# Optimization experiments

Hardware: AMD Instinct MI355X
Metric: run time of the kernel (lower is better)

Reference implementation:

```python
import jax, jax.numpy as jnp
import numpy as np

B_BOUND = 3.0
K = 10
SCALE_DIM = 8
TOTAL_DIM = 16
HID = 50
N = 262144
TD = TOTAL_DIM - SCALE_DIM  # transform_dim


def setup_inputs() -> dict:
    key = jax.random.key(0)
    ks = jax.random.split(key, 7)
    s = 0.1  # small init so softmax/softplus params stay well-conditioned
    return {
        "x": jax.random.normal(ks[0], (N, TOTAL_DIM), dtype=jnp.float32),
        "w0": s * jax.random.normal(ks[1], (SCALE_DIM, HID), dtype=jnp.float32),
        "b0": jnp.zeros((HID,), jnp.float32),
        "w1": s * jax.random.normal(ks[2], (HID, HID), dtype=jnp.float32),
        "b1": jnp.zeros((HID,), jnp.float32),
        "ww": s * jax.random.normal(ks[3], (HID, TD * K), dtype=jnp.float32),
        "bw": jnp.zeros((TD * K,), jnp.float32),
        "wh": s * jax.random.normal(ks[4], (HID, TD * K), dtype=jnp.float32),
        "bh": jnp.zeros((TD * K,), jnp.float32),
        "wd": s * jax.random.normal(ks[5], (HID, TD * (K - 1)), dtype=jnp.float32),
        "bd": jnp.zeros((TD * (K - 1),), jnp.float32),
    }


def _spline_forward(x, w0, b0, w1, b1, ww, bw, wh, bh, wd, bd):
    B = B_BOUND
    zd = x[:, :SCALE_DIM]          # conditioner input [N, d]
    u = x[:, SCALE_DIM:]           # values to transform [N, D]
    n, D = u.shape

    h = jnp.tanh(zd @ w0 + b0)
    h = jnp.tanh(h @ w1 + b1)

    theta_w = jax.nn.softmax((2.0 * B * (h @ ww + bw)).reshape(n, D, K), axis=-1)
    theta_h = jax.nn.softmax((2.0 * B * (h @ wh + bh)).reshape(n, D, K), axis=-1)
    theta_d = jax.nn.softplus((h @ wd + bd).reshape(n, D, K - 1))

    # Bin edges in [-B, B] via cumsum of normalized widths/heights
    xe = jnp.concatenate(
        [jnp.full((n, D, 1), -B, u.dtype), -B + 2.0 * B * jnp.cumsum(theta_w, axis=-1)], axis=-1)  # [n,D,K+1]
    ye = jnp.concatenate(
        [jnp.full((n, D, 1), -B, u.dtype), -B + 2.0 * B * jnp.cumsum(theta_h, axis=-1)], axis=-1)
    # Knot derivatives: boundary derivatives fixed to 1 (linear tails)
    ones = jnp.ones((n, D, 1), u.dtype)
    d = jnp.concatenate([ones, theta_d, ones], axis=-1)  # [n,D,K+1]

    widths = xe[..., 1:] - xe[..., :-1]
    heights = ye[..., 1:] - ye[..., :-1]

    inside = (u > -B) & (u < B)
    uc = jnp.clip(u, -B, B)
    # per-element bin search
    idx = jnp.clip(jnp.sum((uc[..., None] >= xe[..., :-1]).astype(jnp.int32), axis=-1) - 1, 0, K - 1)
    idx = idx[..., None]
    take = lambda a: jnp.take_along_axis(a, idx, axis=-1)[..., 0]

    xk, yk = take(xe[..., :-1]), take(ye[..., :-1])
    wk, hk = take(widths), take(heights)
    dk, dk1 = take(d[..., :-1]), take(d[..., 1:])

    sk = hk / wk
    xi = (uc - xk) / wk
    om = 1.0 - xi
    denom = sk + (dk1 + dk - 2.0 * sk) * xi * om
    y = yk + hk * (sk * xi * xi + dk * xi * om) / denom
    logdet = 2.0 * jnp.log(sk) + jnp.log(dk1 * xi * xi + 2.0 * sk * xi * om + dk * om * om) - 2.0 * jnp.log(denom)

    zD = jnp.where(inside, y, u)
    ld = jnp.where(inside, logdet, 0.0)
    return jnp.concatenate([zd, zD], axis=1), jnp.sum(ld)


def reference(x, w0, b0, w1, b1, ww, bw, wh, bh, wd, bd):
    return _spline_forward(x, w0, b0, w1, b1, ww, bw, wh, bh, wd, bd)
```

## Files before the change

kernel.cpp:

```cpp
#include <hip/hip_runtime.h>

#define NROWS 262144
#define KK 10
#define BB 3.0f
#define SROW 260
#define SEGF16 (16 * SROW)

typedef _Float16 v8h __attribute__((ext_vector_type(8)));
typedef _Float16 v4h __attribute__((ext_vector_type(4)));
typedef float v4f __attribute__((ext_vector_type(4)));

#define W0_OFF 0
#define W1_OFF 256
#define WC_OFF 768
#define FRAG_TOTAL 2816
#define SLOTS_OFF (FRAG_TOTAL * 4)

__device__ __forceinline__ float fast_tanh(float a) {
    float e = __expf(2.0f * a);
    return 1.0f - __fdividef(2.0f, e + 1.0f);
}

__global__ __launch_bounds__(256) void nsf_prep(
    const float* __restrict__ w0, const float* __restrict__ b0,
    const float* __restrict__ w1, const float* __restrict__ b1,
    const float* __restrict__ ww, const float* __restrict__ bw,
    const float* __restrict__ wh, const float* __restrict__ bh,
    const float* __restrict__ wd, const float* __restrict__ bd,
    v8h* __restrict__ wsv, float* __restrict__ wsf)
{
    const int t = blockIdx.x * 256 + threadIdx.x;
    if (t < 64) wsf[SLOTS_OFF + t] = 0.0f;
    if (t >= FRAG_TOTAL) return;

    v8h v;
    #pragma unroll
    for (int j = 0; j < 8; ++j) v[j] = (_Float16)0.0f;

    if (t < W1_OFF) {
        const int tile = t >> 6, lane = t & 63, q = lane >> 4, n = tile * 16 + (lane & 15);
        if (n < 50) {
            #pragma unroll
            for (int j = 0; j < 8; ++j) {
                const int k = q * 8 + j;
                if (k < 8)       v[j] = (_Float16)w0[k * 50 + n];
                else if (k == 8) v[j] = (_Float16)b0[n];
            }
        }
    } else if (t < WC_OFF) {
        int p = t - W1_OFF;
        const int step = p >> 8; p &= 255;
        const int tile = p >> 6, lane = p & 63, q = lane >> 4, n = tile * 16 + (lane & 15);
        if (n < 50) {
            #pragma unroll
            for (int j = 0; j < 8; ++j) {
                const int k = step * 32 + q * 8 + j;
                if (k < 50)       v[j] = (_Float16)w1[k * 50 + n];
                else if (k == 50) v[j] = (_Float16)b1[n];
            }
        }
    } else {
        int p = t - WC_OFF;
        const int step = p >> 10; p &= 1023;
        const int tile = p >> 6, lane = p & 63, q = lane >> 4;
        const int cp = tile * 16 + (lane & 15);
        const int d = cp >> 5, jj = cp & 31;
        #pragma unroll
        for (int j = 0; j < 8; ++j) {
            const int k = step * 32 + q * 8 + j;
            float val = 0.0f;
            if (k < 50) {
                if (jj < 10)      val = ww[k * 80 + d * 10 + jj];
                else if (jj < 20) val = wh[k * 80 + d * 10 + (jj - 10)];
                else if (jj < 29) val = wd[k * 72 + d * 9 + (jj - 20)];
            } else if (k == 50) {
                if (jj < 10)      val = bw[d * 10 + jj];
                else if (jj < 20) val = bh[d * 10 + (jj - 10)];
                else if (jj < 29) val = bd[d * 9 + (jj - 20)];
            }
            v[j] = (_Float16)val;
        }
    }
    wsv[t] = v;
}

__global__ __launch_bounds__(64, 2) void nsf_main(
    const float* __restrict__ x,
    const v8h* __restrict__ wsv,
    float* __restrict__ out, float* __restrict__ slots)
{
    __shared__ __align__(16) _Float16 smem[2 * SEGF16];
    const int lane = threadIdx.x & 63;
    const int q = lane >> 4, l15 = lane & 15;
    _Float16* segA = &smem[0];
    _Float16* segB = &smem[SEGF16];
    const int R0 = blockIdx.x * 32;

    const float4* xv = (const float4*)x;
    float4* ov = (float4*)out;

    const float uA0 = x[(R0 + l15) * 16 + 8 + q];
    const float uA1 = x[(R0 + l15) * 16 + 12 + q];
    const float uB0 = x[(R0 + 16 + l15) * 16 + 8 + q];
    const float uB1 = x[(R0 + 16 + l15) * 16 + 12 + q];

    {
        const int gg = R0 + (lane >> 1);
        const int part = lane & 1;
        ov[gg * 4 + part] = xv[gg * 4 + part];
    }

    v8h aA, aB;
    #pragma unroll
    for (int j = 0; j < 8; ++j) { aA[j] = (_Float16)0.0f; aB[j] = (_Float16)0.0f; }
    if (lane < 16) {
        const float4 f0 = xv[(R0 + lane) * 4 + 0];
        const float4 f1 = xv[(R0 + lane) * 4 + 1];
        aA[0] = (_Float16)f0.x; aA[1] = (_Float16)f0.y; aA[2] = (_Float16)f0.z; aA[3] = (_Float16)f0.w;
        aA[4] = (_Float16)f1.x; aA[5] = (_Float16)f1.y; aA[6] = (_Float16)f1.z; aA[7] = (_Float16)f1.w;
        const float4 g0 = xv[(R0 + 16 + lane) * 4 + 0];
        const float4 g1 = xv[(R0 + 16 + lane) * 4 + 1];
        aB[0] = (_Float16)g0.x; aB[1] = (_Float16)g0.y; aB[2] = (_Float16)g0.z; aB[3] = (_Float16)g0.w;
        aB[4] = (_Float16)g1.x; aB[5] = (_Float16)g1.y; aB[6] = (_Float16)g1.z; aB[7] = (_Float16)g1.w;
    }
    if (q == 1) { aA[0] = (_Float16)1.0f; aB[0] = (_Float16)1.0f; }

    #pragma unroll
    for (int t = 0; t < 4; ++t) {
        const v8h b = wsv[W0_OFF + t * 64 + lane];
        v4f cA = __builtin_amdgcn_mfma_f32_16x16x32_f16(aA, b, (v4f)(0.0f), 0, 0, 0);
        v4f cB = __builtin_amdgcn_mfma_f32_16x16x32_f16(aB, b, (v4f)(0.0f), 0, 0, 0);
        const int n = t * 16 + l15;
        #pragma unroll
        for (int rg = 0; rg < 4; ++rg) {
            segA[(q * 4 + rg) * 72 + n] = (_Float16)fast_tanh(cA[rg]);
            segB[(q * 4 + rg) * 72 + n] = (_Float16)fast_tanh(cB[rg]);
        }
    }

    v8h A0A, A1A, A0B, A1B;
    {
        A0A = *(const v8h*)&segA[l15 * 72 + q * 8];
        A1A = *(const v8h*)&segA[l15 * 72 + 32 + q * 8];
        A0B = *(const v8h*)&segB[l15 * 72 + q * 8];
        A1B = *(const v8h*)&segB[l15 * 72 + 32 + q * 8];
        if (q == 2) { A1A[2] = (_Float16)1.0f; A1B[2] = (_Float16)1.0f; }
        #pragma unroll
        for (int t = 0; t < 4; ++t) {
            const v8h bf0 = wsv[W1_OFF + t * 64 + lane];
            const v8h bf1 = wsv[W1_OFF + 256 + t * 64 + lane];
            v4f cA = __builtin_amdgcn_mfma_f32_16x16x32_f16(A0A, bf0, (v4f)(0.0f), 0, 0, 0);
            cA = __builtin_amdgcn_mfma_f32_16x16x32_f16(A1A, bf1, cA, 0, 0, 0);
            v4f cB = __builtin_amdgcn_mfma_f32_16x16x32_f16(A0B, bf0, (v4f)(0.0f), 0, 0, 0);
            cB = __builtin_amdgcn_mfma_f32_16x16x32_f16(A1B, bf1, cB, 0, 0, 0);
            const int n = t * 16 + l15;
            #pragma unroll
            for (int rg = 0; rg < 4; ++rg) {
                segA[(q * 4 + rg) * 72 + n] = (_Float16)fast_tanh(cA[rg]);
                segB[(q * 4 + rg) * 72 + n] = (_Float16)fast_tanh(cB[rg]);
            }
        }
    }

    {
        A0A = *(const v8h*)&segA[l15 * 72 + q * 8];
        A1A = *(const v8h*)&segA[l15 * 72 + 32 + q * 8];
        A0B = *(const v8h*)&segB[l15 * 72 + q * 8];
        A1B = *(const v8h*)&segB[l15 * 72 + 32 + q * 8];
        if (q == 2) { A1A[2] = (_Float16)1.0f; A1B[2] = (_Float16)1.0f; }
        #pragma unroll 2
        for (int t = 0; t < 16; ++t) {
            const v8h bf0 = wsv[WC_OFF + t * 64 + lane];
            const v8h bf1 = wsv[WC_OFF + 1024 + t * 64 + lane];
            v4f cA = __builtin_amdgcn_mfma_f32_16x16x32_f16(A0A, bf0, (v4f)(0.0f), 0, 0, 0);
            cA = __builtin_amdgcn_mfma_f32_16x16x32_f16(A1A, bf1, cA, 0, 0, 0);
            v4f cB = __builtin_amdgcn_mfma_f32_16x16x32_f16(A0B, bf0, (v4f)(0.0f), 0, 0, 0);
            cB = __builtin_amdgcn_mfma_f32_16x16x32_f16(A1B, bf1, cB, 0, 0, 0);
            const int cp = t * 16 + l15;
            #pragma unroll
            for (int rg = 0; rg < 4; ++rg) {
                segA[(q * 4 + rg) * SROW + cp] = (_Float16)cA[rg];
                segB[(q * 4 + rg) * SROW + cp] = (_Float16)cB[rg];
            }
        }
    }

    float ldacc = 0.0f;
    #pragma unroll 1
    for (int task = 0; task < 4; ++task) {
        const int tile = task >> 1, tt = task & 1;
        const int d = q + tt * 4;
        const int g = R0 + tile * 16 + l15;
        const float ud = (tile == 0) ? (tt == 0 ? uA0 : uA1) : (tt == 0 ? uB0 : uB1);
        const _Float16* sg = (tile == 0) ? segA : segB;
        const int base = l15 * SROW + d * 32;

        float vals[32];
        #pragma unroll
        for (int blk = 0; blk < 8; ++blk) {
            const v4h p = *(const v4h*)&sg[base + blk * 4];
            vals[4 * blk + 0] = (float)p[0];
            vals[4 * blk + 1] = (float)p[1];
            vals[4 * blk + 2] = (float)p[2];
            vals[4 * blk + 3] = (float)p[3];
        }

        float mw = vals[0];
        #pragma unroll
        for (int i = 1; i < KK; ++i) mw = fmaxf(mw, vals[i]);
        float sw = 0.0f;
        #pragma unroll
        for (int i = 0; i < KK; ++i) { vals[i] = __expf(6.0f * (vals[i] - mw)); sw += vals[i]; }
        const float invw = __fdividef(1.0f, sw);

        float mh = vals[10];
        #pragma unroll
        for (int i = 1; i < KK; ++i) mh = fmaxf(mh, vals[10 + i]);
        float sh = 0.0f;
        #pragma unroll
        for (int i = 0; i < KK; ++i) { vals[10 + i] = __expf(6.0f * (vals[10 + i] - mh)); sh += vals[10 + i]; }
        const float invh = __fdividef(1.0f, sh);

        float sp[KK - 1];
        #pragma unroll
        for (int i = 0; i < KK - 1; ++i) {
            const float v = vals[20 + i];
            sp[i] = fmaxf(v, 0.0f) + __logf(1.0f + __expf(-fabsf(v)));
        }

        const float uc = fminf(fmaxf(ud, -BB), BB);
        const bool inside = (ud > -BB) && (ud < BB);

        float cw = 0.0f, ch = 0.0f;
        float xprev = -BB, yprev = -BB, dprev = 1.0f;
        float xk = -BB, yk = -BB, wk = 1.0f, hk2 = 1.0f, dk = 1.0f, dk1 = 1.0f;
        #pragma unroll
        for (int i = 0; i < KK; ++i) {
            cw += vals[i] * invw;
            ch += vals[10 + i] * invh;
            const float xnext = fmaf(6.0f, cw, -BB);
            const float ynext = fmaf(6.0f, ch, -BB);
            const float dnext = (i == KK - 1) ? 1.0f : sp[i];
            const bool c = (i == 0) || (uc >= xprev);
            if (c) { xk = xprev; yk = yprev; wk = xnext - xprev; hk2 = ynext - yprev; dk = dprev; dk1 = dnext; }
            xprev = xnext; yprev = ynext; dprev = dnext;
        }

        const float sk = __fdividef(hk2, wk);
        const float xi = __fdividef(uc - xk, wk);
        const float om = 1.0f - xi;
        const float denom = sk + (dk1 + dk - 2.0f * sk) * xi * om;
        const float ynum = sk * xi * xi + dk * xi * om;
        const float yv = yk + hk2 * __fdividef(ynum, denom);
        const float larg = dk1 * xi * xi + 2.0f * sk * xi * om + dk * om * om;
        const float ldet = 2.0f * __logf(sk) + __logf(larg) - 2.0f * __logf(denom);

        out[g * 16 + 8 + d] = inside ? yv : ud;
        ldacc += inside ? ldet : 0.0f;
    }

    #pragma unroll
    for (int off = 32; off > 0; off >>= 1) ldacc += __shfl_down(ldacc, off);
    if (lane == 0) atomicAdd(&slots[blockIdx.x & 63], ldacc);
}

__global__ void nsf_finish(const float* __restrict__ slots, float* __restrict__ ldp) {
    float v = slots[threadIdx.x];
    #pragma unroll
    for (int off = 32; off > 0; off >>= 1) v += __shfl_down(v, off);
    if (threadIdx.x == 0) *ldp = v;
}

extern "C" void kernel_launch(void* const* d_in, const int* in_sizes, int n_in,
                              void* d_out, int out_size, void* d_ws, size_t ws_size,
                              hipStream_t stream) {
    const float* x  = (const float*)d_in[0];
    const float* w0 = (const float*)d_in[1];
    const float* b0 = (const float*)d_in[2];
    const float* w1 = (const float*)d_in[3];
    const float* b1 = (const float*)d_in[4];
    const float* ww = (const float*)d_in[5];
    const float* bw = (const float*)d_in[6];
    const float* wh = (const float*)d_in[7];
    const float* bh = (const float*)d_in[8];
    const float* wd = (const float*)d_in[9];
    const float* bd = (const float*)d_in[10];

    float* out = (float*)d_out;
    float* ldp = out + (size_t)NROWS * 16;
    v8h* wsv = (v8h*)d_ws;
    float* wsf = (float*)d_ws;
    float* slots = wsf + SLOTS_OFF;

    hipLaunchKernelGGL(nsf_prep, dim3((FRAG_TOTAL + 255) / 256), dim3(256), 0, stream,
                       w0, b0, w1, b1, ww, bw, wh, bh, wd, bd, wsv, wsf);
    hipLaunchKernelGGL(nsf_main, dim3(NROWS / 32), dim3(64), 0, stream,
                       x, wsv, out, slots);
    hipLaunchKernelGGL(nsf_finish, dim3(1), dim3(64), 0, stream, slots, ldp);
}
```

Before: 169.7 us.

## Defer softplus to selected knots, merge logs, fold finish kernel into main

The spline loop now carries the raw derivative logits and applies softplus only to the two selected knots, not to all nine. Boundary knots use a sentinel whose softplus equals 1. The three log calls are merged into one log of a product, and divisions become reciprocal multiplies. The separate finish kernel is replaced by a last-block-done counter inside the main kernel, which saves a launch. The costs are an extra global atomic per block and some risk of precision loss or overflow in the combined log argument.

```diff
diff --git a/kernel.cpp b/kernel.cpp
--- a/kernel.cpp
+++ b/kernel.cpp
@@ -5,6 +5,8 @@
 #define BB 3.0f
 #define SROW 260
 #define SEGF16 (16 * SROW)
+#define NBLOCKS (NROWS / 32)
+#define SENT 0.54132485f
 
 typedef _Float16 v8h __attribute__((ext_vector_type(8)));
 typedef _Float16 v4h __attribute__((ext_vector_type(4)));
@@ -19,6 +21,10 @@
 __device__ __forceinline__ float fast_tanh(float a) {
     float e = __expf(2.0f * a);
     return 1.0f - __fdividef(2.0f, e + 1.0f);
+}
+
+__device__ __forceinline__ float softplus1(float v) {
+    return fmaxf(v, 0.0f) + __logf(1.0f + __expf(-fabsf(v)));
 }
 
 __global__ __launch_bounds__(256) void nsf_prep(
@@ -30,7 +36,7 @@
     v8h* __restrict__ wsv, float* __restrict__ wsf)
 {
     const int t = blockIdx.x * 256 + threadIdx.x;
-    if (t < 64) wsf[SLOTS_OFF + t] = 0.0f;
+    if (t < 65) wsf[SLOTS_OFF + t] = 0.0f;
     if (t >= FRAG_TOTAL) return;
 
     v8h v;
@@ -87,7 +93,7 @@
 __global__ __launch_bounds__(64, 2) void nsf_main(
     const float* __restrict__ x,
     const v8h* __restrict__ wsv,
-    float* __restrict__ out, float* __restrict__ slots)
+    float* __restrict__ out, float* __restrict__ slots, float* __restrict__ ldp)
 {
     __shared__ __align__(16) _Float16 smem[2 * SEGF16];
     const int lane = threadIdx.x & 63;
@@ -221,39 +227,36 @@
         for (int i = 0; i < KK; ++i) { vals[10 + i] = __expf(6.0f * (vals[10 + i] - mh)); sh += vals[10 + i]; }
         const float invh = __fdividef(1.0f, sh);
 
-        float sp[KK - 1];
-        #pragma unroll
-        for (int i = 0; i < KK - 1; ++i) {
-            const float v = vals[20 + i];
-            sp[i] = fmaxf(v, 0.0f) + __logf(1.0f + __expf(-fabsf(v)));
-        }
-
         const float uc = fminf(fmaxf(ud, -BB), BB);
         const bool inside = (ud > -BB) && (ud < BB);
 
         float cw = 0.0f, ch = 0.0f;
-        float xprev = -BB, yprev = -BB, dprev = 1.0f;
-        float xk = -BB, yk = -BB, wk = 1.0f, hk2 = 1.0f, dk = 1.0f, dk1 = 1.0f;
+        float xprev = -BB, yprev = -BB, rprev = SENT;
+        float xk = -BB, yk = -BB, wk = 1.0f, hk2 = 1.0f, rdk = SENT, rdk1 = SENT;
         #pragma unroll
         for (int i = 0; i < KK; ++i) {
             cw += vals[i] * invw;
             ch += vals[10 + i] * invh;
             const float xnext = fmaf(6.0f, cw, -BB);
             const float ynext = fmaf(6.0f, ch, -BB);
-            const float dnext = (i == KK - 1) ? 1.0f : sp[i];
+            const float rnext = (i == KK - 1) ? SENT : vals[20 + i];
             const bool c = (i == 0) || (uc >= xprev);
-            if (c) { xk = xprev; yk = yprev; wk = xnext - xprev; hk2 = ynext - yprev; dk = dprev; dk1 = dnext; }
-            xprev = xnext; yprev = ynext; dprev = dnext;
-        }
-
-        const float sk = __fdividef(hk2, wk);
-        const float xi = __fdividef(uc - xk, wk);
+            if (c) { xk = xprev; yk = yprev; wk = xnext - xprev; hk2 = ynext - yprev; rdk = rprev; rdk1 = rnext; }
+            xprev = xnext; yprev = ynext; rprev = rnext;
+        }
+        const float dk = softplus1(rdk);
+        const float dk1 = softplus1(rdk1);
+
+        const float rwk = __fdividef(1.0f, wk);
+        const float sk = hk2 * rwk;
+        const float xi = (uc - xk) * rwk;
         const float om = 1.0f - xi;
         const float denom = sk + (dk1 + dk - 2.0f * sk) * xi * om;
+        const float rden = __fdividef(1.0f, denom);
         const float ynum = sk * xi * xi + dk * xi * om;
-        const float yv = yk + hk2 * __fdividef(ynum, denom);
+        const float yv = yk + hk2 * ynum * rden;
         const float larg = dk1 * xi * xi + 2.0f * sk * xi * om + dk * om * om;
-        const float ldet = 2.0f * __logf(sk) + __logf(larg) - 2.0f * __logf(denom);
+        const float ldet = __logf(sk * sk * larg * rden * rden);
 
         out[g * 16 + 8 + d] = inside ? yv : ud;
         ldacc += inside ? ldet : 0.0f;
@@ -261,14 +264,20 @@
 
     #pragma unroll
     for (int off = 32; off > 0; off >>= 1) ldacc += __shfl_down(ldacc, off);
-    if (lane == 0) atomicAdd(&slots[blockIdx.x & 63], ldacc);
-}
-
-__global__ void nsf_finish(const float* __restrict__ slots, float* __restrict__ ldp) {
-    float v = slots[threadIdx.x];
-    #pragma unroll
-    for (int off = 32; off > 0; off >>= 1) v += __shfl_down(v, off);
-    if (threadIdx.x == 0) *ldp = v;
+    unsigned int old = 0;
+    if (lane == 0) {
+        atomicAdd(&slots[blockIdx.x & 63], ldacc);
+        __threadfence();
+        old = atomicAdd((unsigned int*)(slots + 64), 1u);
+    }
+    old = (unsigned int)__shfl((int)old, 0);
+    if (old == NBLOCKS - 1) {
+        __threadfence();
+        float v = atomicAdd(&slots[lane], 0.0f);
+        #pragma unroll
+        for (int off = 32; off > 0; off >>= 1) v += __shfl_down(v, off);
+        if (lane == 0) *ldp = v;
+    }
 }
 
 extern "C" void kernel_launch(void* const* d_in, const int* in_sizes, int n_in,
@@ -294,7 +303,6 @@
 
     hipLaunchKernelGGL(nsf_prep, dim3((FRAG_TOTAL + 255) / 256), dim3(256), 0, stream,
                        w0, b0, w1, b1, ww, bw, wh, bh, wd, bd, wsv, wsf);
-    hipLaunchKernelGGL(nsf_main, dim3(NROWS / 32), dim3(64), 0, stream,
-                       x, wsv, out, slots);
-    hipLaunchKernelGGL(nsf_finish, dim3(1), dim3(64), 0, stream, slots, ldp);
-}
+    hipLaunchKernelGGL(nsf_main, dim3(NBLOCKS), dim3(64), 0, stream,
+                       x, wsv, out, slots, ldp);
+}
```

Result: slower. 341.8 us (+101.4%).
